# Performance work log

Measured on AMD Instinct MI355X. Metric: run time of the kernel, lower is better.

Reference implementation:

```python
import jax, jax.numpy as jnp
import numpy as np

B, S, D, H = 2, 2048, 1024, 16
MASK_VAL = -50000.0

def setup_inputs() -> dict:
    key = jax.random.key(0)
    k1, k2, k3, k4 = jax.random.split(key, 4)
    # weights stored as [in, out] so projection is x @ W (equals torch Linear with W.T)
    s = 1.0 / np.sqrt(D)
    return {
        "x": jax.random.normal(k1, (B, S, D), dtype=jnp.float32),
        "Wq": jax.random.normal(k2, (D, D), dtype=jnp.float32) * s,
        "Wkv": jax.random.normal(k3, (D, 2 * D), dtype=jnp.float32) * s,
        "Wo": jax.random.normal(k4, (D, D), dtype=jnp.float32) * s,
    }

def reference(x, Wq, Wkv, Wo):
    b, sl, d = x.shape
    h = H
    hd = d // h
    scale = hd ** (-0.5)
    q = x @ Wq                      # [b, sl, d]
    kv = x @ Wkv                    # [b, sl, 2d]
    k, v = jnp.split(kv, 2, axis=-1)
    # [b, h, s, hd]
    q = q.reshape(b, sl, h, hd).transpose(0, 2, 1, 3)
    k = k.reshape(b, sl, h, hd).transpose(0, 2, 1, 3)
    v = v.reshape(b, sl, h, hd).transpose(0, 2, 1, 3)
    dots = jnp.einsum('bhid,bhjd->bhij', q * scale, k)  # [b,h,s,s]
    # causal: strictly-upper-triangular entries set to MASK_VAL
    causal = jnp.tril(jnp.ones((sl, sl), dtype=bool))
    dots = jnp.where(causal, dots, MASK_VAL)
    attn = jax.nn.softmax(dots, axis=-1)
    out = jnp.einsum('bhij,bhjd->bihd', attn, v).reshape(b, sl, d)
    return out @ Wo
```

## Files before the change

kernel.cpp:

```cpp
#include <hip/hip_runtime.h>

typedef __bf16 bf16_t;
typedef unsigned short u16;
typedef __attribute__((ext_vector_type(8))) __bf16 bf16x8;
typedef __attribute__((ext_vector_type(4))) float f32x4;
typedef __attribute__((ext_vector_type(4))) u16 u16x4;
typedef __attribute__((ext_vector_type(8))) u16 u16x8;

#define SS 2048
#define PSTR 72

__device__ __forceinline__ u16 f2b(float f) {
    return __builtin_bit_cast(u16, (__bf16)f);
}

__device__ __forceinline__ float fexp2(float x) {
#if __has_builtin(__builtin_amdgcn_exp2f)
    return __builtin_amdgcn_exp2f(x);
#else
    float r;
    asm("v_exp_f32 %0, %1" : "=v"(r) : "v"(x));
    return r;
#endif
}

__device__ __forceinline__ void async_copy16(const u16* g, u16* l) {
    __builtin_amdgcn_global_load_lds(
        (__attribute__((address_space(1))) void*)(u16*)g,
        (__attribute__((address_space(3))) void*)l, 16, 0, 0);
}

__device__ __forceinline__ bf16x8 ldfrag(const u16* p) {
    return __builtin_bit_cast(bf16x8, *(const u16x8*)p);
}

__global__ __launch_bounds__(256)
void cast_x_kernel(const float* __restrict__ x, u16* __restrict__ xb) {
    size_t i = ((size_t)blockIdx.x * 256 + threadIdx.x) * 8;
    float4 a = *(const float4*)(x + i);
    float4 b = *(const float4*)(x + i + 4);
    u16x8 o;
    o[0] = f2b(a.x); o[1] = f2b(a.y); o[2] = f2b(a.z); o[3] = f2b(a.w);
    o[4] = f2b(b.x); o[5] = f2b(b.y); o[6] = f2b(b.z); o[7] = f2b(b.w);
    *(u16x8*)(xb + i) = o;
}

__global__ __launch_bounds__(256)
void transpose_all(const float* __restrict__ Wq, const float* __restrict__ Wkv,
                   const float* __restrict__ Wo, u16* __restrict__ WcatT,
                   u16* __restrict__ WoT) {
    const int z = blockIdx.z;
    if (z != 1 && blockIdx.y >= 16) return;
    const float* src; u16* dst; int N; float scale;
    if (z == 0)      { src = Wq;  dst = WcatT;               N = 1024; scale = 0.125f * 1.44269504089f; }
    else if (z == 1) { src = Wkv; dst = WcatT + 1024 * 1024; N = 2048; scale = 1.0f; }
    else             { src = Wo;  dst = WoT;                 N = 1024; scale = 1.0f; }
    __shared__ __attribute__((aligned(16))) u16 tile[64][72];
    const int k0 = blockIdx.x * 64, n0 = blockIdx.y * 64;
    const int tid = threadIdx.x;
#pragma unroll
    for (int p = 0; p < 4; ++p) {
        int c = p * 256 + tid;
        int r = c >> 4, c4 = c & 15;
        float4 v = *(const float4*)(src + (size_t)(k0 + r) * N + n0 + c4 * 4);
        u16x4 o;
        o[0] = f2b(v.x * scale); o[1] = f2b(v.y * scale);
        o[2] = f2b(v.z * scale); o[3] = f2b(v.w * scale);
        *(u16x4*)&tile[r][c4 * 4] = o;
    }
    __syncthreads();
#pragma unroll
    for (int p = 0; p < 4; ++p) {
        int c = p * 256 + tid;
        int n = c >> 4, k4 = c & 15;
        u16x4 o;
#pragma unroll
        for (int i = 0; i < 4; ++i) o[i] = tile[k4 * 4 + i][n];
        *(u16x4*)(dst + (size_t)(n0 + n) * 1024 + k0 + k4 * 4) = o;
    }
}

__global__ __launch_bounds__(256)
void transpose_v(const u16* __restrict__ QKV, u16* __restrict__ VTg) {
    __shared__ __attribute__((aligned(16))) u16 tile[64][72];
    const int s0 = blockIdx.x * 64;
    const int bh = blockIdx.y;
    const int b = bh >> 4, h = bh & 15;
    const int tid = threadIdx.x;
    const u16* src = QKV + ((size_t)b * SS + s0) * 3072 + 2048 + h * 64;
#pragma unroll
    for (int p = 0; p < 4; ++p) {
        int c = p * 256 + tid;
        int s = c >> 4, h4 = c & 15;
        *(u16x4*)&tile[s][h4 * 4] = *(const u16x4*)(src + (size_t)s * 3072 + h4 * 4);
    }
    __syncthreads();
    u16* dst = VTg + (size_t)bh * 64 * 2048 + s0;
#pragma unroll
    for (int p = 0; p < 4; ++p) {
        int c = p * 256 + tid;
        int hd = c >> 4, s4 = c & 15;
        u16x4 o;
#pragma unroll
        for (int i = 0; i < 4; ++i) o[i] = tile[s4 * 4 + i][hd];
        *(u16x4*)(dst + (size_t)hd * 2048 + s4 * 4) = o;
    }
}

template <typename OutT>
__global__ __launch_bounds__(256, 3)
void gemm_bt(const u16* __restrict__ A, const u16* __restrict__ BT,
             OutT* __restrict__ C, int M, int N, int K) {
    __shared__ __attribute__((aligned(16))) u16 As[2][128 * 32];
    __shared__ __attribute__((aligned(16))) u16 Bs[2][128 * 32];
    const int tid = threadIdx.x;
    const int wave = tid >> 6, lane = tid & 63;
    const int l15 = lane & 15, quad = lane >> 4;
    const int m0 = blockIdx.y * 128, n0 = blockIdx.x * 128;
    const int wm = (wave >> 1) * 64, wn = (wave & 1) * 64;
    const f32x4 zero = {0.f, 0.f, 0.f, 0.f};
    f32x4 acc[4][4];
#pragma unroll
    for (int i = 0; i < 4; ++i)
#pragma unroll
        for (int j = 0; j < 4; ++j) acc[i][j] = zero;
    const int r0 = tid >> 2, kc = (tid & 3) * 8;
    auto stage = [&](int bsel, int k0) {
        async_copy16(A + (size_t)(m0 + r0) * K + k0 + kc, As[bsel] + tid * 8);
        async_copy16(BT + (size_t)(n0 + r0) * K + k0 + kc, Bs[bsel] + tid * 8);
        async_copy16(A + (size_t)(m0 + 64 + r0) * K + k0 + kc, As[bsel] + (256 + tid) * 8);
        async_copy16(BT + (size_t)(n0 + 64 + r0) * K + k0 + kc, Bs[bsel] + (256 + tid) * 8);
    };
    stage(0, 0);
    __syncthreads();
    const int nk = K >> 5;
    for (int t = 0; t < nk; ++t) {
        if (t + 1 < nk) stage((t + 1) & 1, (t + 1) * 32);
        const u16* Ab = As[t & 1];
        const u16* Bb = Bs[t & 1];
        bf16x8 af[4], bf[4];
#pragma unroll
        for (int s = 0; s < 4; ++s) {
            af[s] = ldfrag(Ab + (wm + s * 16 + l15) * 32 + quad * 8);
            bf[s] = ldfrag(Bb + (wn + s * 16 + l15) * 32 + quad * 8);
        }
#pragma unroll
        for (int mt = 0; mt < 4; ++mt)
#pragma unroll
            for (int nt = 0; nt < 4; ++nt)
                acc[mt][nt] = __builtin_amdgcn_mfma_f32_16x16x32_bf16(
                    af[mt], bf[nt], acc[mt][nt], 0, 0, 0);
        __syncthreads();
    }
#pragma unroll
    for (int mt = 0; mt < 4; ++mt)
#pragma unroll
        for (int nt = 0; nt < 4; ++nt) {
            const int n = n0 + wn + nt * 16 + l15;
#pragma unroll
            for (int r = 0; r < 4; ++r) {
                const int m = m0 + wm + mt * 16 + quad * 4 + r;
                float v = acc[mt][nt][r];
                if constexpr (sizeof(OutT) == 2) C[(size_t)m * N + n] = (OutT)f2b(v);
                else                             C[(size_t)m * N + n] = v;
            }
        }
}

__global__ __launch_bounds__(256, 2)
void gemm_bt64(const u16* __restrict__ A, const u16* __restrict__ BT,
               float* __restrict__ C, int M, int N, int K) {
    __shared__ __attribute__((aligned(16))) u16 As[2][128 * 32];
    __shared__ __attribute__((aligned(16))) u16 Bs[2][64 * 32];
    const int tid = threadIdx.x;
    const int wave = tid >> 6, lane = tid & 63;
    const int l15 = lane & 15, quad = lane >> 4;
    const int m0 = blockIdx.y * 128, n0 = blockIdx.x * 64;
    const int wm = (wave >> 1) * 64, wn = (wave & 1) * 32;
    const f32x4 zero = {0.f, 0.f, 0.f, 0.f};
    f32x4 acc[4][2];
#pragma unroll
    for (int i = 0; i < 4; ++i)
#pragma unroll
        for (int j = 0; j < 2; ++j) acc[i][j] = zero;
    const int r0 = tid >> 2, kc = (tid & 3) * 8;
    auto stage = [&](int bsel, int k0) {
        async_copy16(A + (size_t)(m0 + r0) * K + k0 + kc, As[bsel] + tid * 8);
        async_copy16(A + (size_t)(m0 + 64 + r0) * K + k0 + kc, As[bsel] + (256 + tid) * 8);
        async_copy16(BT + (size_t)(n0 + r0) * K + k0 + kc, Bs[bsel] + tid * 8);
    };
    stage(0, 0);
    __syncthreads();
    const int nk = K >> 5;
    for (int t = 0; t < nk; ++t) {
        if (t + 1 < nk) stage((t + 1) & 1, (t + 1) * 32);
        const u16* Ab = As[t & 1];
        const u16* Bb = Bs[t & 1];
        bf16x8 af[4], bf[2];
#pragma unroll
        for (int s = 0; s < 4; ++s)
            af[s] = ldfrag(Ab + (wm + s * 16 + l15) * 32 + quad * 8);
#pragma unroll
        for (int s = 0; s < 2; ++s)
            bf[s] = ldfrag(Bb + (wn + s * 16 + l15) * 32 + quad * 8);
#pragma unroll
        for (int mt = 0; mt < 4; ++mt)
#pragma unroll
            for (int nt = 0; nt < 2; ++nt)
                acc[mt][nt] = __builtin_amdgcn_mfma_f32_16x16x32_bf16(
                    af[mt], bf[nt], acc[mt][nt], 0, 0, 0);
        __syncthreads();
    }
#pragma unroll
    for (int mt = 0; mt < 4; ++mt)
#pragma unroll
        for (int nt = 0; nt < 2; ++nt) {
            const int n = n0 + wn + nt * 16 + l15;
#pragma unroll
            for (int r = 0; r < 4; ++r) {
                const int m = m0 + wm + mt * 16 + quad * 4 + r;
                C[(size_t)m * N + n] = acc[mt][nt][r];
            }
        }
}

__device__ __forceinline__ void attn_scoreT(
    const bf16x8 (&kf)[2], const bf16x8 (&qf)[4][2],
    float (&l_i)[4], u16* __restrict__ P, bool diag, int w16, int l15, int quad) {
    const f32x4 cinit = {-10.f, -10.f, -10.f, -10.f};
#pragma unroll
    for (int t = 0; t < 4; ++t) {
        f32x4 a = __builtin_amdgcn_mfma_f32_16x16x32_bf16(kf[0], qf[t][0], cinit, 0, 0, 0);
        f32x4 s = __builtin_amdgcn_mfma_f32_16x16x32_bf16(kf[1], qf[t][1], a, 0, 0, 0);
        if (diag) {
#pragma unroll
            for (int r = 0; r < 4; ++r)
                if (w16 + quad * 4 + r > t * 16 + l15) s[r] = -1e30f;
        }
        u16x4 pk;
        float acc = 0.f;
#pragma unroll
        for (int r = 0; r < 4; ++r) {
            float pv = fexp2(s[r]);
            acc += pv;
            pk[r] = f2b(pv);
        }
        l_i[t] += acc;
        *(u16x4*)(P + (t * 16 + l15) * PSTR + w16 + quad * 4) = pk;
    }
}

__device__ __forceinline__ void attn_pv(
    const u16* __restrict__ P, const bf16x8 (&vf)[4][2],
    f32x4 (&O)[4], int l15, int quad) {
    bf16x8 pf0 = ldfrag(P + l15 * PSTR + quad * 8);
    bf16x8 pf1 = ldfrag(P + l15 * PSTR + 32 + quad * 8);
#pragma unroll
    for (int nt = 0; nt < 4; ++nt) {
        O[nt] = __builtin_amdgcn_mfma_f32_16x16x32_bf16(pf0, vf[nt][0], O[nt], 0, 0, 0);
        O[nt] = __builtin_amdgcn_mfma_f32_16x16x32_bf16(pf1, vf[nt][1], O[nt], 0, 0, 0);
    }
}

__global__ __launch_bounds__(256, 2)
void attn_kernel(const u16* __restrict__ QKV, const u16* __restrict__ VTg,
                 u16* __restrict__ AO) {
    __shared__ __attribute__((aligned(16))) u16 Kt[2][2 * 64 * 32];
    __shared__ __attribute__((aligned(16))) u16 Vt[2][2 * 64 * 32];
    __shared__ __attribute__((aligned(16))) u16 Pq[128 * PSTR];
    const int tid = threadIdx.x;
    const int wave = tid >> 6, lane = tid & 63;
    const int l15 = lane & 15, quad = lane >> 4;
    const int w16 = wave * 16;
    const int bh = blockIdx.y, b = bh >> 4, h = bh & 15;
    const int xe = b ? 15 - (int)blockIdx.x : (int)blockIdx.x;
    const int qbA = 31 - xe, qbB = xe;
    const int qA0 = qbA * 64, qB0 = qbB * 64;
    const size_t bS = (size_t)b * SS;
    const u16* vbase = VTg + (size_t)bh * 64 * 2048;
    const int rr = (tid >> 2) & 63, kc8 = (tid & 3) * 8;

    {
        const u16* qsrcA = QKV + (bS + qA0 + rr) * 3072 + h * 64 + kc8;
        async_copy16(qsrcA,      Pq + tid * 8);
        async_copy16(qsrcA + 32, Pq + (256 + tid) * 8);
        const u16* qsrcB = QKV + (bS + qB0 + rr) * 3072 + h * 64 + kc8;
        async_copy16(qsrcB,      Pq + (512 + tid) * 8);
        async_copy16(qsrcB + 32, Pq + (768 + tid) * 8);
        const u16* ksrc = QKV + (bS + rr) * 3072 + 1024 + h * 64 + kc8;
        async_copy16(ksrc,      Kt[0] + tid * 8);
        async_copy16(ksrc + 32, Kt[0] + (256 + tid) * 8);
        const u16* vsrc = vbase + (size_t)rr * 2048 + kc8;
        async_copy16(vsrc,      Vt[0] + tid * 8);
        async_copy16(vsrc + 32, Vt[0] + (256 + tid) * 8);
    }
    __syncthreads();
    bf16x8 qfA[4][2], qfB[4][2];
#pragma unroll
    for (int t = 0; t < 4; ++t)
#pragma unroll
        for (int ks = 0; ks < 2; ++ks) {
            qfA[t][ks] = ldfrag(Pq + ks * 2048 + (t * 16 + l15) * 32 + quad * 8);
            qfB[t][ks] = ldfrag(Pq + 4096 + ks * 2048 + (t * 16 + l15) * 32 + quad * 8);
        }
    __syncthreads();

    u16* PA = Pq;
    u16* PB = Pq + 64 * PSTR;
    float lA[4], lB[4];
    f32x4 OA[4], OB[4];
    const f32x4 zero = {0.f, 0.f, 0.f, 0.f};
#pragma unroll
    for (int t = 0; t < 4; ++t) { lA[t] = lB[t] = 0.f; }
#pragma unroll
    for (int nt = 0; nt < 4; ++nt) { OA[nt] = zero; OB[nt] = zero; }

    for (int j = 0; j <= qbA; ++j) {
        if (j < qbA) {
            const int kv1 = (j + 1) * 64;
            const int nb = (j + 1) & 1;
            const u16* ksrc = QKV + (bS + kv1 + rr) * 3072 + 1024 + h * 64 + kc8;
            async_copy16(ksrc,      Kt[nb] + tid * 8);
            async_copy16(ksrc + 32, Kt[nb] + (256 + tid) * 8);
            const u16* vsrc = vbase + (size_t)rr * 2048 + kv1 + kc8;
            async_copy16(vsrc,      Vt[nb] + tid * 8);
            async_copy16(vsrc + 32, Vt[nb] + (256 + tid) * 8);
        }
        const bool bAct = (j <= qbB);
        const u16* KB = Kt[j & 1];
        const u16* VB = Vt[j & 1];
        bf16x8 kf[2];
#pragma unroll
        for (int ks = 0; ks < 2; ++ks)
            kf[ks] = ldfrag(KB + ks * 2048 + (w16 + l15) * 32 + quad * 8);
        attn_scoreT(kf, qfA, lA, PA, j == qbA, w16, l15, quad);
        if (bAct)
            attn_scoreT(kf, qfB, lB, PB, j == qbB, w16, l15, quad);
        __syncthreads();
        bf16x8 vf[4][2];
#pragma unroll
        for (int nt = 0; nt < 4; ++nt)
#pragma unroll
            for (int ks = 0; ks < 2; ++ks)
                vf[nt][ks] = ldfrag(VB + ks * 2048 + (nt * 16 + l15) * 32 + quad * 8);
        attn_pv(PA + w16 * PSTR, vf, OA, l15, quad);
        if (bAct)
            attn_pv(PB + w16 * PSTR, vf, OB, l15, quad);
        __syncthreads();
    }

    float* lsh = (float*)Kt;
#pragma unroll
    for (int t = 0; t < 4; ++t) {
        float sA = lA[t];
        sA += __shfl_xor(sA, 16); sA += __shfl_xor(sA, 32);
        float sB = lB[t];
        sB += __shfl_xor(sB, 16); sB += __shfl_xor(sB, 32);
        if (lane < 16) {
            lsh[(t * 16 + l15) * 4 + wave] = sA;
            lsh[(64 + t * 16 + l15) * 4 + wave] = sB;
        }
    }
    __syncthreads();
#pragma unroll
    for (int r = 0; r < 4; ++r) {
        const int qlA = w16 + quad * 4 + r;
        f32x4 la = *(const f32x4*)&lsh[qlA * 4];
        f32x4 lb = *(const f32x4*)&lsh[(64 + qlA) * 4];
        float invA = 1.0f / (la[0] + la[1] + la[2] + la[3]);
        float invB = 1.0f / (lb[0] + lb[1] + lb[2] + lb[3]);
        size_t rowA = bS + (size_t)qA0 + qlA;
        size_t rowB = bS + (size_t)qB0 + qlA;
#pragma unroll
        for (int nt = 0; nt < 4; ++nt) {
            AO[rowA * 1024 + h * 64 + nt * 16 + l15] = f2b(OA[nt][r] * invA);
            AO[rowB * 1024 + h * 64 + nt * 16 + l15] = f2b(OB[nt][r] * invB);
        }
    }
}

extern "C" void kernel_launch(void* const* d_in, const int* in_sizes, int n_in,
                              void* d_out, int out_size, void* d_ws, size_t ws_size,
                              hipStream_t stream) {
    (void)in_sizes; (void)n_in; (void)out_size; (void)ws_size;
    const float* x   = (const float*)d_in[0];
    const float* Wq  = (const float*)d_in[1];
    const float* Wkv = (const float*)d_in[2];
    const float* Wo  = (const float*)d_in[3];
    float* out = (float*)d_out;
    char* ws = (char*)d_ws;
    u16* xb    = (u16*)(ws);
    u16* WcatT = (u16*)(ws + (size_t)(8 << 20));
    u16* WoT   = (u16*)(ws + (size_t)(14 << 20));
    u16* QKV   = (u16*)(ws + (size_t)(16 << 20));
    u16* VTb   = (u16*)(ws + (size_t)(40 << 20));
    u16* AO    = xb;

    cast_x_kernel<<<2048, 256, 0, stream>>>(x, xb);
    transpose_all<<<dim3(16, 32, 3), 256, 0, stream>>>(Wq, Wkv, Wo, WcatT, WoT);
    gemm_bt<u16><<<dim3(24, 32), 256, 0, stream>>>(xb, WcatT, QKV, 4096, 3072, 1024);
    transpose_v<<<dim3(32, 32), 256, 0, stream>>>(QKV, VTb);
    attn_kernel<<<dim3(16, 32), 256, 0, stream>>>(QKV, VTb, AO);
    gemm_bt64<<<dim3(16, 32), 256, 0, stream>>>(AO, WoT, out, 4096, 1024, 1024);
}
```

Measured before the change: 184.6 us.

## Keep attention probabilities in registers by permuting V^T columns, dropping LDS P buffer

Each wave now owns 16 query rows and computes the full 64-key score tile for them, so the probabilities stay in registers and feed the PV MFMA directly without a round trip through shared memory. To make the register layout match the MFMA operand layout, the V transpose kernel writes columns in a permuted order within each 64-key block. This removes the P shared buffer, one __syncthreads per iteration and the cross-wave row-sum reduction through LDS. Q fragments are loaded straight from global memory. In exchange, each wave now reads all K fragments from LDS instead of only its own slice.

```diff
diff --git a/kernel.cpp b/kernel.cpp
--- a/kernel.cpp
+++ b/kernel.cpp
@@ -8,7 +8,6 @@
 typedef __attribute__((ext_vector_type(8))) u16 u16x8;
 
 #define SS 2048
-#define PSTR 72
 
 __device__ __forceinline__ u16 f2b(float f) {
     return __builtin_bit_cast(u16, (__bf16)f);
@@ -103,7 +102,9 @@
         u16x4 o;
 #pragma unroll
         for (int i = 0; i < 4; ++i) o[i] = tile[s4 * 4 + i][hd];
-        *(u16x4*)(dst + (size_t)hd * 2048 + s4 * 4) = o;
+        const int sb = s4 * 4;
+        const int col = (sb & 32) | ((sb & 12) << 1) | ((sb >> 2) & 4);
+        *(u16x4*)(dst + (size_t)hd * 2048 + col) = o;
     }
 }
 
@@ -224,50 +225,11 @@
         }
 }
 
-__device__ __forceinline__ void attn_scoreT(
-    const bf16x8 (&kf)[2], const bf16x8 (&qf)[4][2],
-    float (&l_i)[4], u16* __restrict__ P, bool diag, int w16, int l15, int quad) {
-    const f32x4 cinit = {-10.f, -10.f, -10.f, -10.f};
-#pragma unroll
-    for (int t = 0; t < 4; ++t) {
-        f32x4 a = __builtin_amdgcn_mfma_f32_16x16x32_bf16(kf[0], qf[t][0], cinit, 0, 0, 0);
-        f32x4 s = __builtin_amdgcn_mfma_f32_16x16x32_bf16(kf[1], qf[t][1], a, 0, 0, 0);
-        if (diag) {
-#pragma unroll
-            for (int r = 0; r < 4; ++r)
-                if (w16 + quad * 4 + r > t * 16 + l15) s[r] = -1e30f;
-        }
-        u16x4 pk;
-        float acc = 0.f;
-#pragma unroll
-        for (int r = 0; r < 4; ++r) {
-            float pv = fexp2(s[r]);
-            acc += pv;
-            pk[r] = f2b(pv);
-        }
-        l_i[t] += acc;
-        *(u16x4*)(P + (t * 16 + l15) * PSTR + w16 + quad * 4) = pk;
-    }
-}
-
-__device__ __forceinline__ void attn_pv(
-    const u16* __restrict__ P, const bf16x8 (&vf)[4][2],
-    f32x4 (&O)[4], int l15, int quad) {
-    bf16x8 pf0 = ldfrag(P + l15 * PSTR + quad * 8);
-    bf16x8 pf1 = ldfrag(P + l15 * PSTR + 32 + quad * 8);
-#pragma unroll
-    for (int nt = 0; nt < 4; ++nt) {
-        O[nt] = __builtin_amdgcn_mfma_f32_16x16x32_bf16(pf0, vf[nt][0], O[nt], 0, 0, 0);
-        O[nt] = __builtin_amdgcn_mfma_f32_16x16x32_bf16(pf1, vf[nt][1], O[nt], 0, 0, 0);
-    }
-}
-
 __global__ __launch_bounds__(256, 2)
 void attn_kernel(const u16* __restrict__ QKV, const u16* __restrict__ VTg,
                  u16* __restrict__ AO) {
     __shared__ __attribute__((aligned(16))) u16 Kt[2][2 * 64 * 32];
     __shared__ __attribute__((aligned(16))) u16 Vt[2][2 * 64 * 32];
-    __shared__ __attribute__((aligned(16))) u16 Pq[128 * PSTR];
     const int tid = threadIdx.x;
     const int wave = tid >> 6, lane = tid & 63;
     const int l15 = lane & 15, quad = lane >> 4;
@@ -281,12 +243,6 @@
     const int rr = (tid >> 2) & 63, kc8 = (tid & 3) * 8;
 
     {
-        const u16* qsrcA = QKV + (bS + qA0 + rr) * 3072 + h * 64 + kc8;
-        async_copy16(qsrcA,      Pq + tid * 8);
-        async_copy16(qsrcA + 32, Pq + (256 + tid) * 8);
-        const u16* qsrcB = QKV + (bS + qB0 + rr) * 3072 + h * 64 + kc8;
-        async_copy16(qsrcB,      Pq + (512 + tid) * 8);
-        async_copy16(qsrcB + 32, Pq + (768 + tid) * 8);
         const u16* ksrc = QKV + (bS + rr) * 3072 + 1024 + h * 64 + kc8;
         async_copy16(ksrc,      Kt[0] + tid * 8);
         async_copy16(ksrc + 32, Kt[0] + (256 + tid) * 8);
@@ -294,26 +250,20 @@
         async_copy16(vsrc,      Vt[0] + tid * 8);
         async_copy16(vsrc + 32, Vt[0] + (256 + tid) * 8);
     }
-    __syncthreads();
-    bf16x8 qfA[4][2], qfB[4][2];
-#pragma unroll
-    for (int t = 0; t < 4; ++t)
-#pragma unroll
-        for (int ks = 0; ks < 2; ++ks) {
-            qfA[t][ks] = ldfrag(Pq + ks * 2048 + (t * 16 + l15) * 32 + quad * 8);
-            qfB[t][ks] = ldfrag(Pq + 4096 + ks * 2048 + (t * 16 + l15) * 32 + quad * 8);
-        }
-    __syncthreads();
-
-    u16* PA = Pq;
-    u16* PB = Pq + 64 * PSTR;
-    float lA[4], lB[4];
+    bf16x8 qfA[2], qfB[2];
+    {
+        const u16* qA = QKV + (bS + qA0 + w16 + l15) * 3072 + h * 64 + quad * 8;
+        qfA[0] = ldfrag(qA); qfA[1] = ldfrag(qA + 32);
+        const u16* qB = QKV + (bS + qB0 + w16 + l15) * 3072 + h * 64 + quad * 8;
+        qfB[0] = ldfrag(qB); qfB[1] = ldfrag(qB + 32);
+    }
+    float lA = 0.f, lB = 0.f;
     f32x4 OA[4], OB[4];
     const f32x4 zero = {0.f, 0.f, 0.f, 0.f};
 #pragma unroll
-    for (int t = 0; t < 4; ++t) { lA[t] = lB[t] = 0.f; }
-#pragma unroll
     for (int nt = 0; nt < 4; ++nt) { OA[nt] = zero; OB[nt] = zero; }
+    const f32x4 cinit = {-10.f, -10.f, -10.f, -10.f};
+    __syncthreads();
 
     for (int j = 0; j <= qbA; ++j) {
         if (j < qbA) {
@@ -327,50 +277,92 @@
             async_copy16(vsrc + 32, Vt[nb] + (256 + tid) * 8);
         }
         const bool bAct = (j <= qbB);
+        const bool dA = (j == qbA), dB = (j == qbB);
         const u16* KB = Kt[j & 1];
         const u16* VB = Vt[j & 1];
-        bf16x8 kf[2];
-#pragma unroll
-        for (int ks = 0; ks < 2; ++ks)
-            kf[ks] = ldfrag(KB + ks * 2048 + (w16 + l15) * 32 + quad * 8);
-        attn_scoreT(kf, qfA, lA, PA, j == qbA, w16, l15, quad);
-        if (bAct)
-            attn_scoreT(kf, qfB, lB, PB, j == qbB, w16, l15, quad);
-        __syncthreads();
         bf16x8 vf[4][2];
 #pragma unroll
         for (int nt = 0; nt < 4; ++nt)
 #pragma unroll
             for (int ks = 0; ks < 2; ++ks)
                 vf[nt][ks] = ldfrag(VB + ks * 2048 + (nt * 16 + l15) * 32 + quad * 8);
-        attn_pv(PA + w16 * PSTR, vf, OA, l15, quad);
-        if (bAct)
-            attn_pv(PB + w16 * PSTR, vf, OB, l15, quad);
+        u16x4 pcA[4], pcB[4];
+#pragma unroll
+        for (int c = 0; c < 4; ++c) {
+            bf16x8 kf0 = ldfrag(KB + (c * 16 + l15) * 32 + quad * 8);
+            bf16x8 kf1 = ldfrag(KB + 2048 + (c * 16 + l15) * 32 + quad * 8);
+            f32x4 a = __builtin_amdgcn_mfma_f32_16x16x32_bf16(kf0, qfA[0], cinit, 0, 0, 0);
+            f32x4 s = __builtin_amdgcn_mfma_f32_16x16x32_bf16(kf1, qfA[1], a, 0, 0, 0);
+            if (dA) {
+#pragma unroll
+                for (int r = 0; r < 4; ++r)
+                    if (c * 16 + quad * 4 + r > w16 + l15) s[r] = -1e30f;
+            }
+            u16x4 pk; float acc = 0.f;
+#pragma unroll
+            for (int r = 0; r < 4; ++r) {
+                float pv = fexp2(s[r]);
+                acc += pv;
+                pk[r] = f2b(pv);
+            }
+            lA += acc; pcA[c] = pk;
+            if (bAct) {
+                f32x4 a2 = __builtin_amdgcn_mfma_f32_16x16x32_bf16(kf0, qfB[0], cinit, 0, 0, 0);
+                f32x4 s2 = __builtin_amdgcn_mfma_f32_16x16x32_bf16(kf1, qfB[1], a2, 0, 0, 0);
+                if (dB) {
+#pragma unroll
+                    for (int r = 0; r < 4; ++r)
+                        if (c * 16 + quad * 4 + r > w16 + l15) s2[r] = -1e30f;
+                }
+                u16x4 pk2; float acc2 = 0.f;
+#pragma unroll
+                for (int r = 0; r < 4; ++r) {
+                    float pv = fexp2(s2[r]);
+                    acc2 += pv;
+                    pk2[r] = f2b(pv);
+                }
+                lB += acc2; pcB[c] = pk2;
+            }
+        }
+        bf16x8 paA[2], paB[2];
+#pragma unroll
+        for (int ks = 0; ks < 2; ++ks) {
+            u16x8 t;
+#pragma unroll
+            for (int i = 0; i < 4; ++i) { t[i] = pcA[2 * ks][i]; t[4 + i] = pcA[2 * ks + 1][i]; }
+            paA[ks] = __builtin_bit_cast(bf16x8, t);
+        }
+#pragma unroll
+        for (int nt = 0; nt < 4; ++nt) {
+            OA[nt] = __builtin_amdgcn_mfma_f32_16x16x32_bf16(paA[0], vf[nt][0], OA[nt], 0, 0, 0);
+            OA[nt] = __builtin_amdgcn_mfma_f32_16x16x32_bf16(paA[1], vf[nt][1], OA[nt], 0, 0, 0);
+        }
+        if (bAct) {
+#pragma unroll
+            for (int ks = 0; ks < 2; ++ks) {
+                u16x8 t;
+#pragma unroll
+                for (int i = 0; i < 4; ++i) { t[i] = pcB[2 * ks][i]; t[4 + i] = pcB[2 * ks + 1][i]; }
+                paB[ks] = __builtin_bit_cast(bf16x8, t);
+            }
+#pragma unroll
+            for (int nt = 0; nt < 4; ++nt) {
+                OB[nt] = __builtin_amdgcn_mfma_f32_16x16x32_bf16(paB[0], vf[nt][0], OB[nt], 0, 0, 0);
+                OB[nt] = __builtin_amdgcn_mfma_f32_16x16x32_bf16(paB[1], vf[nt][1], OB[nt], 0, 0, 0);
+            }
+        }
         __syncthreads();
     }
 
-    float* lsh = (float*)Kt;
-#pragma unroll
-    for (int t = 0; t < 4; ++t) {
-        float sA = lA[t];
-        sA += __shfl_xor(sA, 16); sA += __shfl_xor(sA, 32);
-        float sB = lB[t];
-        sB += __shfl_xor(sB, 16); sB += __shfl_xor(sB, 32);
-        if (lane < 16) {
-            lsh[(t * 16 + l15) * 4 + wave] = sA;
-            lsh[(64 + t * 16 + l15) * 4 + wave] = sB;
-        }
-    }
-    __syncthreads();
+    lA += __shfl_xor(lA, 16); lA += __shfl_xor(lA, 32);
+    lB += __shfl_xor(lB, 16); lB += __shfl_xor(lB, 32);
 #pragma unroll
     for (int r = 0; r < 4; ++r) {
-        const int qlA = w16 + quad * 4 + r;
-        f32x4 la = *(const f32x4*)&lsh[qlA * 4];
-        f32x4 lb = *(const f32x4*)&lsh[(64 + qlA) * 4];
-        float invA = 1.0f / (la[0] + la[1] + la[2] + la[3]);
-        float invB = 1.0f / (lb[0] + lb[1] + lb[2] + lb[3]);
-        size_t rowA = bS + (size_t)qA0 + qlA;
-        size_t rowB = bS + (size_t)qB0 + qlA;
+        const int ql = quad * 4 + r;
+        float invA = 1.0f / __shfl(lA, ql);
+        float invB = 1.0f / __shfl(lB, ql);
+        size_t rowA = bS + (size_t)qA0 + w16 + ql;
+        size_t rowB = bS + (size_t)qB0 + w16 + ql;
 #pragma unroll
         for (int nt = 0; nt < 4; ++nt) {
             AO[rowA * 1024 + h * 64 + nt * 16 + l15] = f2b(OA[nt][r] * invA);
```

Measured after the change: 183.2 us. No clear change (-0.8%).
